# Kernel tuning notes

Hardware: AMD Instinct MI355X
Metric: run time of the kernel (lower is better)

The kernel has to match this reference:

```python
import jax, jax.numpy as jnp
import numpy as np

WS = 8   # window_size
SS = 4   # shift_size
NH = 6   # num_heads
EPS = 1e-5


def _win_partition(x, ws):
    # x: [B, H, W, C] -> [B * H/ws * W/ws, ws*ws, C]
    B, H, W, C = x.shape
    x = x.reshape(B, H // ws, ws, W // ws, ws, C)
    return x.transpose(0, 1, 3, 2, 4, 5).reshape(-1, ws * ws, C)


def _win_reverse(wins, ws, H, W, B):
    C = wins.shape[-1]
    x = wins.reshape(B, H // ws, W // ws, ws, ws, C)
    return x.transpose(0, 1, 3, 2, 4, 5).reshape(B, H, W, C)


def _rel_pos_index(ws):
    # static numpy computation, identical to the torch buffer
    coords = np.stack(np.meshgrid(np.arange(ws), np.arange(ws), indexing='ij')).reshape(2, -1)
    rel = coords[:, :, None] - coords[:, None, :]          # [2, N, N]
    rel = rel.transpose(1, 2, 0).copy()                    # [N, N, 2]
    rel[..., 0] += ws - 1
    rel[..., 1] += ws - 1
    rel[..., 0] *= 2 * ws - 1
    return rel.sum(-1)                                     # [N, N] int


def _attn_mask_np(H, W, ws, ss):
    # static numpy computation of the SW-MSA mask, identical to _compute_mask
    img = np.zeros((1, H, W, 1), np.float32)
    cnt = 0
    for hs in (slice(0, -ws), slice(-ws, -ss), slice(-ss, None)):
        for wsl in (slice(0, -ws), slice(-ws, -ss), slice(-ss, None)):
            img[:, hs, wsl, :] = cnt
            cnt += 1
    mw = img.reshape(1, H // ws, ws, W // ws, ws, 1).transpose(0, 1, 3, 2, 4, 5).reshape(-1, ws * ws)
    am = mw[:, None, :] - mw[:, :, None]                   # [nW, N, N]
    return np.where(am != 0, np.float32(-100.0), np.float32(0.0))


def _swin_forward(x, qkv_w, qkv_b, proj_w, proj_b, rpb_table,
                  norm2_g, norm2_b, mlp_w1, mlp_b1, mlp_w2, mlp_b2, H, W):
    B, L, C = x.shape
    ws, ss, nh = WS, SS, NH
    hd = C // nh
    x2d = x.reshape(B, H, W, C)
    shifted = jnp.roll(x2d, (-ss, -ss), axis=(1, 2))
    win = _win_partition(shifted, ws)                      # [B_, N, C]
    B_, N, _ = win.shape

    # --- window attention (note: original applies attention to un-normalized x) ---
    qkv = (win @ qkv_w + qkv_b).reshape(B_, N, 3, nh, hd)
    q = qkv[:, :, 0].transpose(0, 2, 1, 3)                 # [B_, nh, N, hd]
    k = qkv[:, :, 1].transpose(0, 2, 1, 3)
    v = qkv[:, :, 2].transpose(0, 2, 1, 3)
    attn = jnp.einsum('bhnd,bhmd->bhnm', q, k) * (hd ** -0.5)

    bias = rpb_table[jnp.asarray(_rel_pos_index(ws)).reshape(-1)]
    bias = bias.reshape(N, N, nh).transpose(2, 0, 1)       # [nh, N, N]
    attn = attn + bias[None]

    mask = jnp.asarray(_attn_mask_np(H, W, ws, ss))        # [nW, N, N]
    nW = mask.shape[0]
    attn = attn.reshape(B_ // nW, nW, nh, N, N) + mask[None, :, None]
    attn = jax.nn.softmax(attn.reshape(B_, nh, N, N), axis=-1)

    out = jnp.einsum('bhnm,bhmd->bnhd', attn, v).reshape(B_, N, C)
    out = out @ proj_w + proj_b

    x2d = _win_reverse(out, ws, H, W, B)
    x2d = jnp.roll(x2d, (ss, ss), axis=(1, 2))
    x = x + x2d.reshape(B, L, C)

    # --- MLP branch with LayerNorm (norm2) ---
    mu = x.mean(-1, keepdims=True)
    var = x.var(-1, keepdims=True)
    xn = (x - mu) * jax.lax.rsqrt(var + EPS) * norm2_g + norm2_b
    h = jax.nn.gelu(xn @ mlp_w1 + mlp_b1, approximate=False)
    return x + (h @ mlp_w2 + mlp_b2)


def setup_inputs() -> dict:
    B, H, W, C = 8, 128, 128, 192
    mlp_hidden = 4 * C
    ks = jax.random.split(jax.random.key(0), 6)
    std = 0.02
    return {
        'x': jax.random.normal(ks[0], (B, H * W, C), jnp.float32),
        'qkv_w': jax.random.normal(ks[1], (C, 3 * C), jnp.float32) * std,
        'qkv_b': jnp.zeros((3 * C,), jnp.float32),
        'proj_w': jax.random.normal(ks[2], (C, C), jnp.float32) * std,
        'proj_b': jnp.zeros((C,), jnp.float32),
        'rpb_table': jax.random.normal(ks[3], ((2 * WS - 1) ** 2, NH), jnp.float32) * std,
        'norm2_g': jnp.ones((C,), jnp.float32),
        'norm2_b': jnp.zeros((C,), jnp.float32),
        'mlp_w1': jax.random.normal(ks[4], (C, mlp_hidden), jnp.float32) * std,
        'mlp_b1': jnp.zeros((mlp_hidden,), jnp.float32),
        'mlp_w2': jax.random.normal(ks[5], (mlp_hidden, C), jnp.float32) * std,
        'mlp_b2': jnp.zeros((C,), jnp.float32),
        'H': H,
        'W': W,
    }


def reference(x, qkv_w, qkv_b, proj_w, proj_b, rpb_table, norm2_g, norm2_b,
              mlp_w1, mlp_b1, mlp_w2, mlp_b2, H, W):
    return _swin_forward(x, qkv_w, qkv_b, proj_w, proj_b, rpb_table,
                         norm2_g, norm2_b, mlp_w1, mlp_b1, mlp_w2, mlp_b2, H, W)
```

## Files before the change

### kernel.cpp

```cpp
#include <hip/hip_runtime.h>
#include <hip/hip_bf16.h>


typedef __hip_bfloat16 bf16;
typedef __attribute__((ext_vector_type(8))) short bfrag;
typedef __attribute__((ext_vector_type(4))) float ffrag;

union bfu { bf16 h[8]; bfrag v; };

__device__ __forceinline__ float b2f(bf16 v) { return __bfloat162float(v); }
__device__ __forceinline__ bf16  f2b(float v) { return __float2bfloat16(v); }

#define MFMA(a, b, c) __builtin_amdgcn_mfma_f32_16x16x32_bf16((a), (b), (c), 0, 0, 0)

#define WS_XRES  0ULL
#define WS_OG    100663296ULL
#define WS_QKVTG 150994944ULL
#define WS_QBG   151250944ULL
#define WS_PROJT 151253504ULL
#define WS_W1T   151330304ULL
#define WS_W2T   151637504ULL
#define WS_SB    152006144ULL

__device__ __forceinline__ void stage_lds(const void* g, void* l, int nbytes, int t) {
    const int lane16 = (t & 63) * 16;
    for (int base = (t >> 6) * 1024; base < nbytes; base += 4096) {
        if (base + lane16 < nbytes) {
            __builtin_amdgcn_global_load_lds(
                (const __attribute__((address_space(1))) void*)((const char*)g + base + lane16),
                (__attribute__((address_space(3))) void*)((char*)l + base),
                16, 0, 0);
        }
    }
}

__device__ __forceinline__ float gelu_t(float x) {
    float y = x * (1.5957691216057308f + 0.07135481627f * x * x);
    return x * (1.f / (1.f + __expf(-y)));
}

__global__ __launch_bounds__(256) void k_prep(
    const float* __restrict__ qkv_w, const float* __restrict__ qkv_b,
    const float* __restrict__ proj_w, const float* __restrict__ w1,
    const float* __restrict__ w2, const float* __restrict__ rpb,
    char* __restrict__ ws)
{
    int i = blockIdx.x * 256 + threadIdx.x;
    bf16*  qkvTg = (bf16*)(ws + WS_QKVTG);
    float* qbg   = (float*)(ws + WS_QBG);
    bf16*  projT = (bf16*)(ws + WS_PROJT);
    bf16*  w1T   = (bf16*)(ws + WS_W1T);
    bf16*  w2T   = (bf16*)(ws + WS_W2T);
    bf16*  sbB   = (bf16*)(ws + WS_SB);

    if (i < 128000) {
        int g = i / 64000, rem = i % 64000;
        int c = rem / 200, k = rem % 200;
        float v = 0.f;
        if (k < 192) {
            if (c < 96)       v = qkv_w[k * 576 + g * 96 + c];
            else if (c < 192) v = qkv_w[k * 576 + 192 + g * 96 + (c - 96)];
            else if (c < 288) v = qkv_w[k * 576 + 384 + g * 96 + (c - 192)];
        }
        qkvTg[i] = f2b(v);
    } else if (i < 128640) {
        int j = i - 128000;
        int g = j / 320, c = j % 320;
        float v = 0.f;
        if (c < 96)       v = qkv_b[g * 96 + c];
        else if (c < 192) v = qkv_b[192 + g * 96 + (c - 96)];
        else if (c < 288) v = qkv_b[384 + g * 96 + (c - 192)];
        qbg[j] = v;
    } else if (i < 167040) {
        int j = i - 128640;
        int c = j / 200, k = j % 200;
        projT[j] = f2b(k < 192 ? proj_w[k * 192 + c] : 0.f);
    } else if (i < 320640) {
        int j = i - 167040;
        int c = j / 200, k = j % 200;
        w1T[j] = f2b(k < 192 ? w1[k * 768 + c] : 0.f);
    } else if (i < 504960) {
        int j = i - 320640;
        int kc = j / 7680, r = (j % 7680) / 40, kk = j % 40;
        w2T[j] = f2b(kk < 32 ? w2[(kc * 32 + kk) * 192 + r] : 0.f);
    } else if (i < 603264) {
        int j = i - 504960;
        int cls = j / 24576, h = (j % 24576) / 4096;
        int ii = (j % 4096) / 64, jj = j % 64;
        int ri = ii >> 3, ci = ii & 7, rj = jj >> 3, cj = jj & 7;
        float bias = rpb[(((ri - rj + 7) * 15) + (ci - cj + 7)) * 6 + h];
        int clsR = cls >> 1, clsC = cls & 1;
        int regi = (clsR ? (ri < 4 ? 1 : 2) : 0) * 3 + (clsC ? (ci < 4 ? 1 : 2) : 0);
        int regj = (clsR ? (rj < 4 ? 1 : 2) : 0) * 3 + (clsC ? (cj < 4 ? 1 : 2) : 0);
        sbB[j] = f2b(bias + (regi == regj ? 0.f : -100.f));
    }
}

__global__ __launch_bounds__(256, 2) void k_attn(
    const float* __restrict__ x, const char* __restrict__ ws,
    bf16* __restrict__ Og)
{
    __shared__ __align__(16) unsigned char smem[77824];
    bf16*  sWb = (bf16*)(smem);
    bf16*  sQ  = (bf16*)(smem + 25600);
    bf16*  sK  = (bf16*)(smem + 38912);
    bf16*  sVT = (bf16*)(smem + 52224);
    bf16*  sP  = (bf16*)(smem + 66048);
    float* sQB = (float*)(smem + 75264);

    const bf16*  qkvTg = (const bf16*)(ws + WS_QKVTG);
    const float* qbg   = (const float*)(ws + WS_QBG);
    const bf16*  sbB   = (const bf16*)(ws + WS_SB);

    const int t    = threadIdx.x;
    const int lane = t & 63, quad = lane >> 4, l15 = lane & 15;
    const int wave = t >> 6, r0 = wave * 16;
    const int win = blockIdx.x;
    const int b   = win >> 8;
    const int wi  = win & 255;
    const int wh  = wi >> 4, wwi = wi & 15;

    stage_lds(qbg, smem + 75264, 2560, t);
    stage_lds(qkvTg, sWb, 12800, t);

    bfrag aX[6];
    {
        int row = r0 + l15;
        int rr = row >> 3, cc = row & 7;
        int hs  = (wh * 8 + rr + 4) & 127;
        int wsx = (wwi * 8 + cc + 4) & 127;
        const float* xrow = x + ((size_t)(b * 16384 + hs * 128 + wsx)) * 192;
        #pragma unroll
        for (int kb = 0; kb < 6; kb++) {
            float4 f0 = *(const float4*)(xrow + kb * 32 + quad * 8);
            float4 f1 = *(const float4*)(xrow + kb * 32 + quad * 8 + 4);
            bfu u;
            u.h[0] = f2b(f0.x); u.h[1] = f2b(f0.y); u.h[2] = f2b(f0.z); u.h[3] = f2b(f0.w);
            u.h[4] = f2b(f1.x); u.h[5] = f2b(f1.y); u.h[6] = f2b(f1.z); u.h[7] = f2b(f1.w);
            aX[kb] = u.v;
        }
    }

    const int cls = ((wh == 15) ? 2 : 0) + ((wwi == 15) ? 1 : 0);
    const bf16* bBc = sbB + (size_t)cls * 24576;
    bf16* sPw = sP + wave * 16 * 72;

    __syncthreads();

    int pb = 0;
    for (int g = 0; g < 2; g++) {
        for (int c = 0; c < 9; c++) {
            if (c < 8)
                stage_lds(qkvTg + (size_t)(g * 320 + (c + 1) * 32) * 200,
                          sWb + (pb ^ 1) * 6400, 12800, t);
            else if (g == 0)
                stage_lds(qkvTg + (size_t)320 * 200,
                          sWb + (pb ^ 1) * 6400, 12800, t);
            const bf16* sW = sWb + pb * 6400;
            #pragma unroll
            for (int ct = 0; ct < 2; ct++) {
                int c0 = c * 32 + ct * 16;
                bfrag bw[6];
                #pragma unroll
                for (int kb = 0; kb < 6; kb++)
                    bw[kb] = *(const bfrag*)&sW[(ct * 16 + l15) * 200 + kb * 32 + quad * 8];
                ffrag acc = {0.f, 0.f, 0.f, 0.f};
                #pragma unroll
                for (int kb = 0; kb < 6; kb++) acc = MFMA(aX[kb], bw[kb], acc);
                float bias = sQB[g * 320 + c0 + l15];
                #pragma unroll
                for (int reg = 0; reg < 4; reg++) {
                    int r = r0 + quad * 4 + reg;
                    float v = acc[reg] + bias;
                    if (c0 < 96)       sQ[r * 104 + c0 + l15] = f2b(v);
                    else if (c0 < 192) sK[r * 104 + (c0 - 96) + l15] = f2b(v);
                    else               sVT[(c0 - 192 + l15) * 72 + r] = f2b(v);
                }
            }
            __syncthreads();
            pb ^= 1;
        }
        for (int hl = 0; hl < 3; hl++) {
            int h = g * 3 + hl;
            bfrag aQ = *(const bfrag*)&sQ[(r0 + l15) * 104 + hl * 32 + quad * 8];
            ffrag Sf[4];
            #pragma unroll
            for (int jt = 0; jt < 4; jt++) {
                bfrag bK = *(const bfrag*)&sK[(jt * 16 + l15) * 104 + hl * 32 + quad * 8];
                ffrag z = {0.f, 0.f, 0.f, 0.f};
                Sf[jt] = MFMA(aQ, bK, z);
            }
            const bf16* bb = bBc + h * 4096 + (r0 + quad * 4) * 64 + l15;
            #pragma unroll
            for (int jt = 0; jt < 4; jt++)
                #pragma unroll
                for (int reg = 0; reg < 4; reg++)
                    Sf[jt][reg] = Sf[jt][reg] * 0.1767766952966369f
                                + b2f(bb[reg * 64 + jt * 16]);
            #pragma unroll
            for (int reg = 0; reg < 4; reg++) {
                float m = fmaxf(fmaxf(Sf[0][reg], Sf[1][reg]), fmaxf(Sf[2][reg], Sf[3][reg]));
                m = fmaxf(m, __shfl_xor(m, 1)); m = fmaxf(m, __shfl_xor(m, 2));
                m = fmaxf(m, __shfl_xor(m, 4)); m = fmaxf(m, __shfl_xor(m, 8));
                float s = 0.f;
                #pragma unroll
                for (int jt = 0; jt < 4; jt++) { Sf[jt][reg] = __expf(Sf[jt][reg] - m); s += Sf[jt][reg]; }
                s += __shfl_xor(s, 1); s += __shfl_xor(s, 2);
                s += __shfl_xor(s, 4); s += __shfl_xor(s, 8);
                float inv = 1.f / s;
                int prow = (quad * 4 + reg) * 72;
                #pragma unroll
                for (int jt = 0; jt < 4; jt++)
                    sPw[prow + jt * 16 + l15] = f2b(Sf[jt][reg] * inv);
            }
            bfrag aP0 = *(const bfrag*)&sPw[l15 * 72 + quad * 8];
            bfrag aP1 = *(const bfrag*)&sPw[l15 * 72 + 32 + quad * 8];
            #pragma unroll
            for (int ct = 0; ct < 2; ct++) {
                bfrag bV0 = *(const bfrag*)&sVT[(hl * 32 + ct * 16 + l15) * 72 + quad * 8];
                bfrag bV1 = *(const bfrag*)&sVT[(hl * 32 + ct * 16 + l15) * 72 + 32 + quad * 8];
                ffrag z = {0.f, 0.f, 0.f, 0.f};
                ffrag o = MFMA(aP1, bV1, MFMA(aP0, bV0, z));
                #pragma unroll
                for (int reg = 0; reg < 4; reg++)
                    Og[((size_t)win * 64 + r0 + quad * 4 + reg) * 192 + h * 32 + ct * 16 + l15]
                        = f2b(o[reg]);
            }
        }
        __syncthreads();
    }
}

__global__ __launch_bounds__(256, 2) void k_proj(
    const float* __restrict__ x, const float* __restrict__ proj_b,
    const char* __restrict__ ws, float* __restrict__ xres)
{
    __shared__ __align__(16) bf16 sWp[192 * 200];

    const bf16* projT = (const bf16*)(ws + WS_PROJT);
    const bf16* Og    = (const bf16*)(ws + WS_OG);

    const int t    = threadIdx.x;
    const int lane = t & 63, quad = lane >> 4, l15 = lane & 15;
    const int wave = t >> 6, r0 = wave * 32;
    const size_t row0 = (size_t)blockIdx.x * 128;

    stage_lds(projT, sWp, 76800, t);

    bfrag aO[2][6];
    #pragma unroll
    for (int rt = 0; rt < 2; rt++)
        #pragma unroll
        for (int kb = 0; kb < 6; kb++)
            aO[rt][kb] = *(const bfrag*)&Og[(row0 + r0 + rt * 16 + l15) * 192 + kb * 32 + quad * 8];

    size_t tokb[2][4];
    #pragma unroll
    for (int rt = 0; rt < 2; rt++)
        #pragma unroll
        for (int reg = 0; reg < 4; reg++) {
            int n = r0 + rt * 16 + quad * 4 + reg;
            int w2 = (int)(blockIdx.x * 2) + (n >> 6);
            int nl = n & 63;
            int b = w2 >> 8, wi = w2 & 255;
            int wh = wi >> 4, wwi = wi & 15;
            int sr = wh * 8 + (nl >> 3), sc = wwi * 8 + (nl & 7);
            int h2 = (sr + 4) & 127, w2c = (sc + 4) & 127;
            tokb[rt][reg] = ((size_t)(b * 16384 + h2 * 128 + w2c)) * 192;
        }

    __syncthreads();

    ffrag acc[2][12];
    #pragma unroll
    for (int rt = 0; rt < 2; rt++)
        #pragma unroll
        for (int ct = 0; ct < 12; ct++)
            acc[rt][ct] = (ffrag){0.f, 0.f, 0.f, 0.f};

    #pragma unroll
    for (int ct = 0; ct < 12; ct++) {
        bfrag bw[6];
        #pragma unroll
        for (int kb = 0; kb < 6; kb++)
            bw[kb] = *(const bfrag*)&sWp[(ct * 16 + l15) * 200 + kb * 32 + quad * 8];
        #pragma unroll
        for (int rt = 0; rt < 2; rt++)
            #pragma unroll
            for (int kb = 0; kb < 6; kb++)
                acc[rt][ct] = MFMA(aO[rt][kb], bw[kb], acc[rt][ct]);
    }

    #pragma unroll
    for (int rt = 0; rt < 2; rt++)
        #pragma unroll
        for (int ct = 0; ct < 12; ct++) {
            int col = ct * 16 + l15;
            float pb = proj_b[col];
            #pragma unroll
            for (int reg = 0; reg < 4; reg++) {
                size_t gi = tokb[rt][reg] + col;
                xres[gi] = acc[rt][ct][reg] + pb + x[gi];
            }
        }
}

__global__ __launch_bounds__(256, 4) void k_mlp(
    const float* __restrict__ xres, const float* __restrict__ g,
    const float* __restrict__ bb, const float* __restrict__ b1,
    const float* __restrict__ b2, const char* __restrict__ ws,
    float* __restrict__ out)
{
    __shared__ __align__(16) unsigned char smem[36352];
    bf16*  w1s  = (bf16*)(smem);
    bf16*  w2s  = (bf16*)(smem + 12800);
    bf16*  hS   = (bf16*)(smem + 28160);
    float* sB1f = (float*)(smem + 33280);
    bf16*  U    = (bf16*)(smem);

    const bf16* w1T = (const bf16*)(ws + WS_W1T);
    const bf16* w2T = (const bf16*)(ws + WS_W2T);

    const int t    = threadIdx.x;
    const int lane = t & 63, quad = lane >> 4, l15 = lane & 15;
    const int wave = t >> 6, r0 = wave * 16;
    const size_t row0 = (size_t)blockIdx.x * 64;

    stage_lds(b1, smem + 33280, 3072, t);

    {
        int row = r0 + l15;
        const float4* src = (const float4*)(xres + (row0 + row) * 192 + quad * 48);
        float v[48];
        float s = 0.f, sq = 0.f;
        #pragma unroll
        for (int u = 0; u < 12; u++) {
            float4 f = src[u];
            v[u*4] = f.x; v[u*4+1] = f.y; v[u*4+2] = f.z; v[u*4+3] = f.w;
            s  += f.x + f.y + f.z + f.w;
            sq += f.x*f.x + f.y*f.y + f.z*f.z + f.w*f.w;
        }
        s  += __shfl_xor(s, 16);  s  += __shfl_xor(s, 32);
        sq += __shfl_xor(sq, 16); sq += __shfl_xor(sq, 32);
        float mean = s * (1.f / 192.f);
        float var  = sq * (1.f / 192.f) - mean * mean;
        float rstd = rsqrtf(var + 1e-5f);
        __hip_bfloat162* dst = (__hip_bfloat162*)&U[row * 200 + quad * 48];
        #pragma unroll
        for (int u = 0; u < 24; u++) {
            int c = quad * 48 + u * 2;
            float a0 = (v[u*2]   - mean) * rstd * g[c]     + bb[c];
            float a1 = (v[u*2+1] - mean) * rstd * g[c + 1] + bb[c + 1];
            dst[u] = __float22bfloat162_rn({a0, a1});
        }
    }
    __syncthreads();

    bfrag aX[6];
    #pragma unroll
    for (int kb = 0; kb < 6; kb++)
        aX[kb] = *(const bfrag*)&U[(r0 + l15) * 200 + kb*32 + quad*8];

    __syncthreads();

    stage_lds(w1T, w1s, 12800, t);
    stage_lds(w2T, (char*)w2s, 15360, t);
    __syncthreads();

    bf16* hs_w = hS + wave * 16 * 40;

    ffrag oacc[12];
    #pragma unroll
    for (int ct = 0; ct < 12; ct++)
        oacc[ct] = (ffrag){0.f, 0.f, 0.f, 0.f};

    for (int kc = 0; kc < 24; kc++) {
        #pragma unroll
        for (int ct = 0; ct < 2; ct++) {
            bfrag bw[6];
            #pragma unroll
            for (int kb = 0; kb < 6; kb++)
                bw[kb] = *(const bfrag*)&w1s[(ct*16 + l15) * 200 + kb*32 + quad*8];
            float bias = sB1f[kc * 32 + ct * 16 + l15];
            ffrag a = {0.f, 0.f, 0.f, 0.f};
            #pragma unroll
            for (int kb = 0; kb < 6; kb++) a = MFMA(aX[kb], bw[kb], a);
            #pragma unroll
            for (int reg = 0; reg < 4; reg++)
                hs_w[(quad*4 + reg) * 40 + ct*16 + l15] =
                    f2b(gelu_t(a[reg] + bias));
        }
        bfrag aH = *(const bfrag*)&hs_w[l15 * 40 + quad*8];
        #pragma unroll
        for (int ct = 0; ct < 12; ct++) {
            bfrag bw2 = *(const bfrag*)&w2s[(ct*16 + l15) * 40 + quad*8];
            oacc[ct] = MFMA(aH, bw2, oacc[ct]);
        }
        __syncthreads();
        if (kc < 23) {
            stage_lds(w1T + (size_t)(kc + 1) * 6400, w1s, 12800, t);
            stage_lds(w2T + (size_t)(kc + 1) * 7680, (char*)w2s, 15360, t);
            __syncthreads();
        }
    }

    #pragma unroll
    for (int ct = 0; ct < 12; ct++) {
        int col = ct * 16 + l15;
        float b2v = b2[col];
        #pragma unroll
        for (int reg = 0; reg < 4; reg++) {
            size_t gi = (row0 + r0 + quad*4 + reg) * 192 + col;
            out[gi] = xres[gi] + oacc[ct][reg] + b2v;
        }
    }
}

extern "C" void kernel_launch(void* const* d_in, const int* in_sizes, int n_in,
                              void* d_out, int out_size, void* d_ws, size_t ws_size,
                              hipStream_t stream)
{
    (void)in_sizes; (void)n_in; (void)out_size; (void)ws_size;

    const float* x      = (const float*)d_in[0];
    const float* qkv_w  = (const float*)d_in[1];
    const float* qkv_b  = (const float*)d_in[2];
    const float* proj_w = (const float*)d_in[3];
    const float* proj_b = (const float*)d_in[4];
    const float* rpb    = (const float*)d_in[5];
    const float* n2g    = (const float*)d_in[6];
    const float* n2b    = (const float*)d_in[7];
    const float* w1     = (const float*)d_in[8];
    const float* b1     = (const float*)d_in[9];
    const float* w2     = (const float*)d_in[10];
    const float* b2     = (const float*)d_in[11];

    char*  ws   = (char*)d_ws;
    float* xres = (float*)(ws + WS_XRES);
    bf16*  Og   = (bf16*)(ws + WS_OG);
    float* out  = (float*)d_out;

    hipLaunchKernelGGL(k_prep, dim3(2357), dim3(256), 0, stream,
                       qkv_w, qkv_b, proj_w, w1, w2, rpb, ws);
    hipLaunchKernelGGL(k_attn, dim3(2048), dim3(256), 0, stream,
                       x, ws, Og);
    hipLaunchKernelGGL(k_proj, dim3(1024), dim3(256), 0, stream,
                       x, proj_b, ws, xres);
    hipLaunchKernelGGL(k_mlp,  dim3(2048), dim3(256), 0, stream,
                       xres, n2g, n2b, b1, b2, ws, out);
}
```

Before: 479.6 us.

## Split fused MLP into two chunked GEMM kernels with whole-weight LDS residency

The fused per-64-row MLP kernel restreamed small slices of W1/W2 through LDS 24 times per block, with a barrier at each step. It is replaced by two kernels run over four row chunks. k_mlp1 does LayerNorm and FC1+GELU, holds a 384-column half of W1 in LDS, and writes the bf16 hidden activations to global memory, reusing the Og workspace. k_mlp2 streams W2 in double-buffered 192-row slices and accumulates FC2 plus the residual. This gives far more reuse of each staged weight, but adds a round trip of the hidden tensor through global memory, extra kernel launches, and very large LDS use that limits each CU to one 512-thread block.

New measurement: 604.2 us. 1.26x slower.

```diff
diff --git a/kernel.cpp b/kernel.cpp
--- a/kernel.cpp
+++ b/kernel.cpp
@@ -25,6 +25,18 @@
 __device__ __forceinline__ void stage_lds(const void* g, void* l, int nbytes, int t) {
     const int lane16 = (t & 63) * 16;
     for (int base = (t >> 6) * 1024; base < nbytes; base += 4096) {
+        if (base + lane16 < nbytes) {
+            __builtin_amdgcn_global_load_lds(
+                (const __attribute__((address_space(1))) void*)((const char*)g + base + lane16),
+                (__attribute__((address_space(3))) void*)((char*)l + base),
+                16, 0, 0);
+        }
+    }
+}
+
+__device__ __forceinline__ void stage_lds8(const void* g, void* l, int nbytes, int t) {
+    const int lane16 = (t & 63) * 16;
+    for (int base = (t >> 6) * 1024; base < nbytes; base += 8192) {
         if (base + lane16 < nbytes) {
             __builtin_amdgcn_global_load_lds(
                 (const __attribute__((address_space(1))) void*)((const char*)g + base + lane16),
@@ -79,12 +91,12 @@
         int j = i - 167040;
         int c = j / 200, k = j % 200;
         w1T[j] = f2b(k < 192 ? w1[k * 768 + c] : 0.f);
-    } else if (i < 504960) {
+    } else if (i < 474240) {
         int j = i - 320640;
-        int kc = j / 7680, r = (j % 7680) / 40, kk = j % 40;
-        w2T[j] = f2b(kk < 32 ? w2[(kc * 32 + kk) * 192 + r] : 0.f);
-    } else if (i < 603264) {
-        int j = i - 504960;
+        int kc = j / 38400, r = (j % 38400) / 200, kk = j % 200;
+        w2T[j] = f2b(kk < 192 ? w2[(kc * 192 + kk) * 192 + r] : 0.f);
+    } else if (i < 572544) {
+        int j = i - 474240;
         int cls = j / 24576, h = (j % 24576) / 4096;
         int ii = (j % 4096) / 64, jj = j % 64;
         int ri = ii >> 3, ci = ii & 7, rj = jj >> 3, cj = jj & 7;
@@ -305,113 +317,141 @@
         }
 }
 
-__global__ __launch_bounds__(256, 4) void k_mlp(
+__global__ __launch_bounds__(512, 2) void k_mlp1(
     const float* __restrict__ xres, const float* __restrict__ g,
     const float* __restrict__ bb, const float* __restrict__ b1,
-    const float* __restrict__ b2, const char* __restrict__ ws,
-    float* __restrict__ out)
-{
-    __shared__ __align__(16) unsigned char smem[36352];
-    bf16*  w1s  = (bf16*)(smem);
-    bf16*  w2s  = (bf16*)(smem + 12800);
-    bf16*  hS   = (bf16*)(smem + 28160);
-    float* sB1f = (float*)(smem + 33280);
-    bf16*  U    = (bf16*)(smem);
+    const char* __restrict__ ws, bf16* __restrict__ hbuf, int row0c)
+{
+    __shared__ __align__(16) bf16 sW1[384 * 200];
 
     const bf16* w1T = (const bf16*)(ws + WS_W1T);
-    const bf16* w2T = (const bf16*)(ws + WS_W2T);
 
     const int t    = threadIdx.x;
     const int lane = t & 63, quad = lane >> 4, l15 = lane & 15;
-    const int wave = t >> 6, r0 = wave * 16;
-    const size_t row0 = (size_t)blockIdx.x * 64;
-
-    stage_lds(b1, smem + 33280, 3072, t);
-
-    {
-        int row = r0 + l15;
-        const float4* src = (const float4*)(xres + (row0 + row) * 192 + quad * 48);
-        float v[48];
+    const int wave = t >> 6, r0 = wave * 32;
+    const int ht = blockIdx.x >> 7, rb = blockIdx.x & 127;
+    const size_t rowb = (size_t)row0c + (size_t)rb * 256;
+
+    stage_lds8(w1T + (size_t)ht * 384 * 200, sW1, 153600, t);
+
+    bfrag aX[2][6];
+    #pragma unroll
+    for (int rt = 0; rt < 2; rt++) {
+        const float* xrow = xres + (rowb + r0 + rt * 16 + l15) * 192;
         float s = 0.f, sq = 0.f;
         #pragma unroll
-        for (int u = 0; u < 12; u++) {
-            float4 f = src[u];
-            v[u*4] = f.x; v[u*4+1] = f.y; v[u*4+2] = f.z; v[u*4+3] = f.w;
-            s  += f.x + f.y + f.z + f.w;
-            sq += f.x*f.x + f.y*f.y + f.z*f.z + f.w*f.w;
+        for (int kb = 0; kb < 6; kb++) {
+            float4 f0 = *(const float4*)(xrow + kb * 32 + quad * 8);
+            float4 f1 = *(const float4*)(xrow + kb * 32 + quad * 8 + 4);
+            s  += f0.x + f0.y + f0.z + f0.w + f1.x + f1.y + f1.z + f1.w;
+            sq += f0.x*f0.x + f0.y*f0.y + f0.z*f0.z + f0.w*f0.w
+                + f1.x*f1.x + f1.y*f1.y + f1.z*f1.z + f1.w*f1.w;
         }
         s  += __shfl_xor(s, 16);  s  += __shfl_xor(s, 32);
         sq += __shfl_xor(sq, 16); sq += __shfl_xor(sq, 32);
         float mean = s * (1.f / 192.f);
         float var  = sq * (1.f / 192.f) - mean * mean;
         float rstd = rsqrtf(var + 1e-5f);
-        __hip_bfloat162* dst = (__hip_bfloat162*)&U[row * 200 + quad * 48];
-        #pragma unroll
-        for (int u = 0; u < 24; u++) {
-            int c = quad * 48 + u * 2;
-            float a0 = (v[u*2]   - mean) * rstd * g[c]     + bb[c];
-            float a1 = (v[u*2+1] - mean) * rstd * g[c + 1] + bb[c + 1];
-            dst[u] = __float22bfloat162_rn({a0, a1});
-        }
-    }
+        #pragma unroll
+        for (int kb = 0; kb < 6; kb++) {
+            int c = kb * 32 + quad * 8;
+            float4 f0 = *(const float4*)(xrow + c);
+            float4 f1 = *(const float4*)(xrow + c + 4);
+            float4 g0 = *(const float4*)(g + c);
+            float4 g1 = *(const float4*)(g + c + 4);
+            float4 c0 = *(const float4*)(bb + c);
+            float4 c1 = *(const float4*)(bb + c + 4);
+            bfu u;
+            u.h[0] = f2b((f0.x - mean) * rstd * g0.x + c0.x);
+            u.h[1] = f2b((f0.y - mean) * rstd * g0.y + c0.y);
+            u.h[2] = f2b((f0.z - mean) * rstd * g0.z + c0.z);
+            u.h[3] = f2b((f0.w - mean) * rstd * g0.w + c0.w);
+            u.h[4] = f2b((f1.x - mean) * rstd * g1.x + c1.x);
+            u.h[5] = f2b((f1.y - mean) * rstd * g1.y + c1.y);
+            u.h[6] = f2b((f1.z - mean) * rstd * g1.z + c1.z);
+            u.h[7] = f2b((f1.w - mean) * rstd * g1.w + c1.w);
+            aX[rt][kb] = u.v;
+        }
+    }
+
     __syncthreads();
 
-    bfrag aX[6];
-    #pragma unroll
-    for (int kb = 0; kb < 6; kb++)
-        aX[kb] = *(const bfrag*)&U[(r0 + l15) * 200 + kb*32 + quad*8];
+    for (int ct = 0; ct < 24; ct++) {
+        bfrag bw[6];
+        #pragma unroll
+        for (int kb = 0; kb < 6; kb++)
+            bw[kb] = *(const bfrag*)&sW1[(ct * 16 + l15) * 200 + kb * 32 + quad * 8];
+        float bias = b1[ht * 384 + ct * 16 + l15];
+        #pragma unroll
+        for (int rt = 0; rt < 2; rt++) {
+            ffrag a = {0.f, 0.f, 0.f, 0.f};
+            #pragma unroll
+            for (int kb = 0; kb < 6; kb++) a = MFMA(aX[rt][kb], bw[kb], a);
+            #pragma unroll
+            for (int reg = 0; reg < 4; reg++) {
+                size_t hr = (size_t)rb * 256 + r0 + rt * 16 + quad * 4 + reg;
+                hbuf[hr * 768 + ht * 384 + ct * 16 + l15] =
+                    f2b(gelu_t(a[reg] + bias));
+            }
+        }
+    }
+}
+
+__global__ __launch_bounds__(512, 2) void k_mlp2(
+    const bf16* __restrict__ hbuf, const float* __restrict__ xres,
+    const float* __restrict__ b2, const char* __restrict__ ws,
+    float* __restrict__ out, int row0c)
+{
+    __shared__ __align__(16) bf16 sW2[2][192 * 200];
+
+    const bf16* w2T = (const bf16*)(ws + WS_W2T);
+
+    const int t    = threadIdx.x;
+    const int lane = t & 63, quad = lane >> 4, l15 = lane & 15;
+    const int wave = t >> 6, r0 = wave * 16;
+    const size_t rowbl = (size_t)blockIdx.x * 128;
+
+    stage_lds8(w2T, sW2[0], 76800, t);
+
+    ffrag acc[12];
+    #pragma unroll
+    for (int ct = 0; ct < 12; ct++)
+        acc[ct] = (ffrag){0.f, 0.f, 0.f, 0.f};
 
     __syncthreads();
 
-    stage_lds(w1T, w1s, 12800, t);
-    stage_lds(w2T, (char*)w2s, 15360, t);
-    __syncthreads();
-
-    bf16* hs_w = hS + wave * 16 * 40;
-
-    ffrag oacc[12];
-    #pragma unroll
-    for (int ct = 0; ct < 12; ct++)
-        oacc[ct] = (ffrag){0.f, 0.f, 0.f, 0.f};
-
-    for (int kc = 0; kc < 24; kc++) {
-        #pragma unroll
-        for (int ct = 0; ct < 2; ct++) {
+    for (int kc = 0; kc < 4; kc++) {
+        if (kc < 3)
+            stage_lds8(w2T + (size_t)(kc + 1) * 38400, sW2[(kc + 1) & 1], 76800, t);
+        const bf16* w2c = sW2[kc & 1];
+
+        bfrag aH[6];
+        #pragma unroll
+        for (int kb = 0; kb < 6; kb++)
+            aH[kb] = *(const bfrag*)&hbuf[(rowbl + r0 + l15) * 768
+                                          + kc * 192 + kb * 32 + quad * 8];
+        #pragma unroll
+        for (int ct = 0; ct < 12; ct++) {
             bfrag bw[6];
             #pragma unroll
             for (int kb = 0; kb < 6; kb++)
-                bw[kb] = *(const bfrag*)&w1s[(ct*16 + l15) * 200 + kb*32 + quad*8];
-            float bias = sB1f[kc * 32 + ct * 16 + l15];
-            ffrag a = {0.f, 0.f, 0.f, 0.f};
-            #pragma unroll
-            for (int kb = 0; kb < 6; kb++) a = MFMA(aX[kb], bw[kb], a);
-            #pragma unroll
-            for (int reg = 0; reg < 4; reg++)
-                hs_w[(quad*4 + reg) * 40 + ct*16 + l15] =
-                    f2b(gelu_t(a[reg] + bias));
-        }
-        bfrag aH = *(const bfrag*)&hs_w[l15 * 40 + quad*8];
-        #pragma unroll
-        for (int ct = 0; ct < 12; ct++) {
-            bfrag bw2 = *(const bfrag*)&w2s[(ct*16 + l15) * 40 + quad*8];
-            oacc[ct] = MFMA(aH, bw2, oacc[ct]);
+                bw[kb] = *(const bfrag*)&w2c[(ct * 16 + l15) * 200 + kb * 32 + quad * 8];
+            #pragma unroll
+            for (int kb = 0; kb < 6; kb++)
+                acc[ct] = MFMA(aH[kb], bw[kb], acc[ct]);
         }
         __syncthreads();
-        if (kc < 23) {
-            stage_lds(w1T + (size_t)(kc + 1) * 6400, w1s, 12800, t);
-            stage_lds(w2T + (size_t)(kc + 1) * 7680, (char*)w2s, 15360, t);
-            __syncthreads();
-        }
-    }
-
+    }
+
+    const size_t rowg = (size_t)row0c + rowbl;
     #pragma unroll
     for (int ct = 0; ct < 12; ct++) {
         int col = ct * 16 + l15;
         float b2v = b2[col];
         #pragma unroll
         for (int reg = 0; reg < 4; reg++) {
-            size_t gi = (row0 + r0 + quad*4 + reg) * 192 + col;
-            out[gi] = xres[gi] + oacc[ct][reg] + b2v;
+            size_t gi = (rowg + r0 + quad * 4 + reg) * 192 + col;
+            out[gi] = xres[gi] + acc[ct][reg] + b2v;
         }
     }
 }
@@ -440,12 +480,16 @@
     bf16*  Og   = (bf16*)(ws + WS_OG);
     float* out  = (float*)d_out;
 
-    hipLaunchKernelGGL(k_prep, dim3(2357), dim3(256), 0, stream,
+    hipLaunchKernelGGL(k_prep, dim3(2237), dim3(256), 0, stream,
                        qkv_w, qkv_b, proj_w, w1, w2, rpb, ws);
     hipLaunchKernelGGL(k_attn, dim3(2048), dim3(256), 0, stream,
                        x, ws, Og);
     hipLaunchKernelGGL(k_proj, dim3(1024), dim3(256), 0, stream,
                        x, proj_b, ws, xres);
-    hipLaunchKernelGGL(k_mlp,  dim3(2048), dim3(256), 0, stream,
-                       xres, n2g, n2b, b1, b2, ws, out);
-}
+    for (int c = 0; c < 4; c++) {
+        hipLaunchKernelGGL(k_mlp1, dim3(256), dim3(512), 0, stream,
+                           xres, n2g, n2b, b1, ws, Og, c * 32768);
+        hipLaunchKernelGGL(k_mlp2, dim3(256), dim3(512), 0, stream,
+                           Og, xres, b2, ws, out, c * 32768);
+    }
+}
```
